# Performance work log

Hardware: AMD Instinct MI355X
Metric: run time of the kernel (lower is better)

Reference implementation:

```python
import jax, jax.numpy as jnp
import numpy as np
from jax import lax

STRIDES = (8, 16, 32)
NUM_CLASSES = 80
TOPK = 1000
CONF_THRESH = 0.05
NMS_THRESH = 0.6


def setup_inputs() -> dict:
    key = jax.random.key(0)
    ks = jax.random.split(key, 10)
    hw = [(256, 256), (128, 128), (64, 64)]
    inp = {}
    for lv, (h, w) in enumerate(hw):
        inp[f"cls_pred_{lv}"] = jax.random.normal(ks[3 * lv + 0], (NUM_CLASSES, h, w), jnp.float32)
        inp[f"reg_pred_{lv}"] = jax.random.normal(ks[3 * lv + 1], (4, h, w), jnp.float32)
        inp[f"ctn_pred_{lv}"] = jax.random.normal(ks[3 * lv + 2], (1, h, w), jnp.float32)
    inp["scales"] = jax.random.uniform(ks[9], (3,), jnp.float32)
    return inp


def _level_decode(cls_p, reg_p, ctn_p, scale, stride):
    # cls_p: [C,H,W] -> flatten to [M,C] matching torch permute(1,2,0).view(-1,C)
    C, H, W = cls_p.shape
    cls = jnp.transpose(cls_p, (1, 2, 0)).reshape(-1, C)          # [M,C]
    reg = jnp.transpose(reg_p, (1, 2, 0)).reshape(-1, 4)          # [M,4]
    reg = jax.nn.relu(reg * scale) * stride                       # Scale + relu + stride
    ctn = jnp.transpose(ctn_p, (1, 2, 0)).reshape(-1, 1)          # [M,1]
    joint = jnp.sqrt(jax.nn.sigmooid(cls) * jax.nn.sigmoid(ctn)) if False else \
        jnp.sqrt(jax.nn.sigmoid(cls) * jax.nn.sigmoid(ctn))      # [M,C]
    scores = jnp.max(joint, axis=-1)                              # [M]
    labels = jnp.argmax(joint, axis=-1)                           # [M]
    ay, ax = jnp.meshgrid(jnp.arange(H), jnp.arange(W), indexing='ij')
    anchors = (jnp.stack([ax, ay], -1).reshape(-1, 2).astype(cls.dtype) + 0.5) * stride  # [M,2]
    # per-level topk (M > TOPK for all levels here)
    scores, idx = lax.top_k(scores, TOPK)
    labels = labels[idx]
    reg = reg[idx]
    anchors = anchors[idx]
    boxes = jnp.concatenate([anchors - reg[:, :2], anchors + reg[:, 2:]], axis=-1)  # x1y1x2y2
    return scores, labels, boxes


def _nms(boxes, scores):
    # Faithful port of the pure-python NMS: fixed-shape keep mask, sorted order.
    N = boxes.shape[0]
    order = jnp.argsort(-scores)
    b = boxes[order]
    x1, y1, x2, y2 = b[:, 0], b[:, 1], b[:, 2], b[:, 3]
    areas = (x2 - x1) * (y2 - y1)
    xx1 = jnp.maximum(x1[:, None], x1[None, :])
    yy1 = jnp.maximum(y1[:, None], y1[None, :])
    xx2 = jnp.minimum(x2[:, None], x2[None, :])
    yy2 = jnp.minimum(y2[:, None], y2[None, :])
    w = jnp.maximum(1e-10, xx2 - xx1)
    h = jnp.maximum(1e-10, yy2 - yy1)
    inter = w * h
    iou = inter / (areas[:, None] + areas[None, :] - inter + 1e-14)  # [N,N]
    idxs = jnp.arange(N)

    def body(i, keep):
        sup = (iou[i] > NMS_THRESH) & (idxs > i) & keep[i]
        return keep & ~sup

    keep = lax.fori_loop(0, N, body, jnp.ones((N,), bool))
    return order, keep


def reference(cls_pred_0, cls_pred_1, cls_pred_2,
              reg_pred_0, reg_pred_1, reg_pred_2,
              ctn_pred_0, ctn_pred_1, ctn_pred_2, scales):
    cls_l = [cls_pred_0, cls_pred_1, cls_pred_2]
    reg_l = [reg_pred_0, reg_pred_1, reg_pred_2]
    ctn_l = [ctn_pred_0, ctn_pred_1, ctn_pred_2]
    all_s, all_l, all_b = [], [], []
    for lv in range(3):
        s, lb, bx = _level_decode(cls_l[lv], reg_l[lv], ctn_l[lv], scales[lv], float(STRIDES[lv]))
        all_s.append(s); all_l.append(lb); all_b.append(bx)
    scores = jnp.concatenate(all_s)   # [3000]
    labels = jnp.concatenate(all_l)
    boxes = jnp.concatenate(all_b)    # [3000,4]
    order, keep = _nms(boxes, scores)
    scores_s = scores[order]
    labels_s = labels[order]
    boxes_s = boxes[order]
    keep = keep & (scores_s > CONF_THRESH)
    return boxes_s, scores_s, labels_s, keep
```

## Files before the change

### kernel.cpp

```cpp
#include <hip/hip_runtime.h>
#include <cmath>
#include <stdint.h>

#define NPTS   86016
#define NB     (1 << 18)
#define NCB    1024
#define K_TOP  1000
#define NOUT   3000
#define NWORDS 47
#define NTILE  47
#define CAND_CAP 16384
#define ECAP   8192
#define FCAP   1024
#define SPPB   64

#define HIST_OFF   0
#define CH_OFF     (NB * 3 * 4)
#define CNT_OFF    (CH_OFF + NCB * 3 * 4)
#define MEMSET_BYTES (CNT_OFF + 64)
#define KEYS_OFF   (CNT_OFF + 64)
#define LAB_OFF    (KEYS_OFF + NPTS * 8)
#define SURE_OFF   (LAB_OFF + NPTS * 4)
#define CAND_OFF   (SURE_OFF + 3 * 1024 * 8)
#define SURV_OFF   (CAND_OFF + 3 * CAND_CAP * 8)
#define EDGE_OFF   (SURV_OFF + NOUT * 8 + 64)
#define FLAG_OFF   (EDGE_OFF + ECAP * 4)

__device__ __forceinline__ float sig_f32_stepwise(float x) {
    float e = (float)exp(-(double)x);
    return 1.0f / (1.0f + e);
}

__device__ __forceinline__ void locate(int g, int& lv, int& p, int& HW) {
    if (g < 65536)      { lv = 0; p = g;         HW = 65536; }
    else if (g < 81920) { lv = 1; p = g - 65536; HW = 16384; }
    else                { lv = 2; p = g - 81920; HW = 4096;  }
}

__global__ __launch_bounds__(256) void score_kernel(
        const float* __restrict__ cls0, const float* __restrict__ cls1,
        const float* __restrict__ cls2,
        const float* __restrict__ ctn0, const float* __restrict__ ctn1,
        const float* __restrict__ ctn2,
        unsigned long long* __restrict__ keys, int* __restrict__ labels,
        int* __restrict__ hist, int* __restrict__ chist,
        int* __restrict__ cnt, unsigned* __restrict__ flags) {
    __shared__ float pm[5 * SPPB], pv[5 * SPPB];
    __shared__ int pidx[5 * SPPB];
    __shared__ int lch[NCB];
    const int tid = threadIdx.x;
    const int base = blockIdx.x * SPPB;
    for (int i = tid; i < NCB; i += 256) lch[i] = 0;
    for (int it = tid; it < 5 * SPPB; it += 256) {
        int c = it / SPPB, pt = it - c * SPPB;
        int g = base + pt, lv, p, HW;
        locate(g, lv, p, HW);
        const float* cls = (lv == 0) ? cls0 : ((lv == 1) ? cls1 : cls2);
        const float* bp = cls + (size_t)c * 16 * HW + p;
        float x[16];
#pragma unroll
        for (int cc = 0; cc < 16; cc++) x[cc] = bp[(size_t)cc * HW];
        float m = -INFINITY, v = -INFINITY; int idx = 0;
#pragma unroll
        for (int cc = 0; cc < 16; cc++)
            if (x[cc] > m) { v = m; m = x[cc]; idx = c * 16 + cc; }
        pm[it] = m; pv[it] = v; pidx[it] = idx;
    }
    __syncthreads();
    if (tid < SPPB) {
        int g = base + tid, lv, p, HW;
        locate(g, lv, p, HW);
        const float* ctn = (lv == 0) ? ctn0 : ((lv == 1) ? ctn1 : ctn2);
        float m = -INFINITY, v = -INFINITY; int idx = 0;
#pragma unroll
        for (int k = 0; k < 5; k++) {
            float bm = pm[k * SPPB + tid];
            float bv = pv[k * SPPB + tid];
            int bidx = pidx[k * SPPB + tid];
            if (bm > m) { v = fmaxf(m, bv); m = bm; idx = bidx; }
        }
        float sc = sig_f32_stepwise(ctn[p]);
        float sM = sig_f32_stepwise(m);
        float jm = __fsqrt_rn(sM * sc);
        float sV = sig_f32_stepwise(v);
        float jv = __fsqrt_rn(sV * sc);
        if (jv == jm) {
            int f = atomicAdd(&cnt[13], 1);
            if (f < FCAP) flags[f] = (unsigned)g;
        }
        unsigned int bits = __float_as_uint(jm);
        keys[g] = ((unsigned long long)bits << 32) | (0xFFFFFFFFu - (unsigned)g);
        labels[g] = idx;
        atomicAdd(&hist[lv * NB + (int)(bits >> 12)], 1);
        atomicAdd(&lch[(int)(bits >> 20)], 1);
    }
    __syncthreads();
    int lv0, p0, HW0; locate(base, lv0, p0, HW0);
    for (int i = tid; i < NCB; i += 256) {
        int v = lch[i];
        if (v) atomicAdd(&chist[lv0 * NCB + i], v);
    }
}

__global__ __launch_bounds__(1024) void thresh_kernel(
        const float* __restrict__ cls0, const float* __restrict__ cls1,
        const float* __restrict__ cls2,
        const float* __restrict__ ctn0, const float* __restrict__ ctn1,
        const float* __restrict__ ctn2,
        const int* __restrict__ hist, const int* __restrict__ chist,
        int* __restrict__ cnt,
        const unsigned* __restrict__ flags, int* __restrict__ labels) {
    int bid = blockIdx.x, tid = threadIdx.x;
    if (bid < 3) {
        int lv = bid;
        const int* h = hist + lv * NB;
        __shared__ int part[1024];
        __shared__ int s_chunk, s_above;
        __shared__ int bins[257];
        part[tid] = chist[lv * NCB + tid];
        __syncthreads();
        for (int off = 1; off < 1024; off <<= 1) {
            int v = part[tid] + ((tid + off < 1024) ? part[tid + off] : 0);
            __syncthreads(); part[tid] = v; __syncthreads();
        }
        int nxt = (tid < 1023) ? part[tid + 1] : 0;
        if (part[tid] >= K_TOP && nxt < K_TOP) { s_chunk = tid; s_above = nxt; }
        __syncthreads();
        int chunk = s_chunk, above = s_above;
        if (tid < 256) bins[tid] = h[chunk * 256 + tid];
        __syncthreads();
        for (int off = 1; off < 256; off <<= 1) {
            int v = 0;
            if (tid < 256) v = bins[tid] + ((tid + off < 256) ? bins[tid + off] : 0);
            __syncthreads(); if (tid < 256) bins[tid] = v; __syncthreads();
        }
        if (tid < 256) {
            int ge    = above + bins[tid];
            int genxt = above + ((tid < 255) ? bins[tid + 1] : 0);
            if (ge >= K_TOP && genxt < K_TOP) {
                cnt[6 + lv] = chunk * 256 + tid;
                cnt[9 + lv] = K_TOP - genxt;
            }
        }
    } else {
        int nf = cnt[13]; if (nf > FCAP) nf = FCAP;
        int wave = tid >> 6, lane = tid & 63;
        for (int f = wave; f < nf; f += 16) {
            int g = (int)flags[f], lv, p, HW;
            locate(g, lv, p, HW);
            const float* cls = (lv == 0) ? cls0 : ((lv == 1) ? cls1 : cls2);
            const float* ctn = (lv == 0) ? ctn0 : ((lv == 1) ? ctn1 : ctn2);
            float sc = sig_f32_stepwise(ctn[p]);
            float bestv = -1.0f; int besti = 127;
            {
                float s = sig_f32_stepwise(cls[(size_t)lane * HW + p]);
                float sj = __fsqrt_rn(s * sc);
                bestv = sj; besti = lane;
            }
            if (lane < 16) {
                int c2 = lane + 64;
                float s = sig_f32_stepwise(cls[(size_t)c2 * HW + p]);
                float sj = __fsqrt_rn(s * sc);
                if (sj > bestv) { bestv = sj; besti = c2; }
            }
            for (int off = 32; off; off >>= 1) {
                float ov = __shfl_xor(bestv, off, 64);
                int   oi = __shfl_xor(besti, off, 64);
                if (ov > bestv || (ov == bestv && oi < besti)) { bestv = ov; besti = oi; }
            }
            if (lane == 0) labels[g] = besti;
        }
    }
}

__global__ void compact_kernel(const unsigned long long* __restrict__ keys,
                               int* __restrict__ cnt,
                               unsigned long long* __restrict__ sure,
                               unsigned long long* __restrict__ cand) {
    int g = blockIdx.x * blockDim.x + threadIdx.x;
    if (g >= NPTS) return;
    int lv = (g < 65536) ? 0 : (g < 81920 ? 1 : 2);
    unsigned long long key = keys[g];
    int bin = (int)(key >> 44);
    int B = cnt[6 + lv];
    if (bin > B) {
        int i = atomicAdd(&cnt[0 + lv], 1);
        sure[lv * 1024 + i] = key;
    } else if (bin == B) {
        int i = atomicAdd(&cnt[3 + lv], 1);
        if (i < CAND_CAP) cand[lv * CAND_CAP + i] = key;
    }
}

__global__ void select_kernel(const int* __restrict__ cnt,
                              const unsigned long long* __restrict__ sure,
                              unsigned long long* __restrict__ cand,
                              unsigned long long* __restrict__ surv) {
    int lv = blockIdx.x, tid = threadIdx.x;
    unsigned long long* c = cand + lv * CAND_CAP;
    int n = cnt[3 + lv]; if (n > CAND_CAP) n = CAND_CAP;
    int R = cnt[9 + lv];
    int Ca = K_TOP - R;
    int m = 1; while (m < n) m <<= 1;
    for (int t = n + tid; t < m; t += 1024) c[t] = 0ULL;
    __syncthreads();
    for (int k = 2; k <= m; k <<= 1)
        for (int j = k >> 1; j > 0; j >>= 1) {
            for (int t = tid; t < m; t += 1024) {
                int l = t ^ j;
                if (l > t) {
                    unsigned long long a = c[t], b = c[l];
                    if (((t & k) == 0) ? (a < b) : (a > b)) { c[t] = b; c[l] = a; }
                }
            }
            __syncthreads();
        }
    __shared__ unsigned long long s[1024];
    s[tid] = (tid < Ca) ? sure[lv * 1024 + tid]
                        : ((tid < K_TOP) ? c[tid - Ca] : 0ULL);
    __syncthreads();
    for (int k = 2; k <= 1024; k <<= 1)
        for (int j = k >> 1; j > 0; j >>= 1) {
            int l = tid ^ j;
            if (l > tid) {
                unsigned long long a = s[tid], b = s[l];
                if (((tid & k) == 0) ? (a < b) : (a > b)) { s[tid] = b; s[l] = a; }
            }
            __syncthreads();
        }
    if (tid < K_TOP) surv[lv * K_TOP + tid] = s[tid];
}

__global__ __launch_bounds__(1024) void merge_emit_kernel(
        const unsigned long long* __restrict__ surv,
        const int* __restrict__ labels,
        const float* __restrict__ reg0, const float* __restrict__ reg1,
        const float* __restrict__ reg2,
        const float* __restrict__ scales,
        float* __restrict__ out) {
    __shared__ unsigned long long L[3][1024];
    __shared__ unsigned long long s[NOUT];
    int tid = threadIdx.x;
#pragma unroll
    for (int lv = 0; lv < 3; lv++)
        L[lv][tid] = (tid < K_TOP) ? surv[lv * K_TOP + tid] : 0ULL;
    __syncthreads();
    for (int e = tid; e < NOUT; e += 1024) {
        int a = e / K_TOP, i = e - a * K_TOP;
        unsigned long long key = L[a][i];
        int rank = i;
#pragma unroll
        for (int b = 0; b < 3; b++) {
            if (b == a) continue;
            int lo = 0, hi = K_TOP;
            while (lo < hi) {
                int mid = (lo + hi) >> 1;
                if (L[b][mid] > key) lo = mid + 1; else hi = mid;
            }
            rank += lo;
        }
        s[rank] = key;
    }
    __syncthreads();
    for (int r = tid; r < NOUT; r += 1024) {
        unsigned long long key = s[r];
        unsigned int bits = (unsigned)(key >> 32);
        float score = __uint_as_float(bits);
        unsigned int g = 0xFFFFFFFFu - (unsigned)(key & 0xFFFFFFFFULL);
        int lv, p;
        if (g < 65536u)      { lv = 0; p = (int)g; }
        else if (g < 81920u) { lv = 1; p = (int)g - 65536; }
        else                 { lv = 2; p = (int)g - 81920; }
        const float* rp = (lv == 0) ? reg0 : ((lv == 1) ? reg1 : reg2);
        int HW = (lv == 0) ? 65536 : ((lv == 1) ? 16384 : 4096);
        int W = 256 >> lv;
        float strideF = (float)(8 << lv);
        float scale = scales[lv];
        int x = p & (W - 1);
        int y = p >> (8 - lv);
        float r0 = fmaxf(0.0f, rp[0 * HW + p] * scale) * strideF;
        float r1 = fmaxf(0.0f, rp[1 * HW + p] * scale) * strideF;
        float r2 = fmaxf(0.0f, rp[2 * HW + p] * scale) * strideF;
        float r3 = fmaxf(0.0f, rp[3 * HW + p] * scale) * strideF;
        float ax = ((float)x + 0.5f) * strideF;
        float ay = ((float)y + 0.5f) * strideF;
        out[r * 4 + 0] = ax - r0;
        out[r * 4 + 1] = ay - r1;
        out[r * 4 + 2] = ax + r2;
        out[r * 4 + 3] = ay + r3;
        out[12000 + r] = score;
        out[15000 + r] = (float)labels[g];
    }
}

__global__ __launch_bounds__(256) void edge_kernel(const float* __restrict__ out,
                                                   unsigned* __restrict__ edges_g,
                                                   int* __restrict__ cnt) {
    __shared__ float x1[128], y1[128], x2[128], y2[128];
    int t = blockIdx.x, tid = threadIdx.x;
    int ta = 0, rem = t;
    while (rem >= NTILE - ta) { rem -= NTILE - ta; ta++; }
    int tb = ta + rem;
    if (tid < 64) {
        int gi = ta * 64 + tid;
        if (gi < NOUT) {
            float4 b = ((const float4*)out)[gi];
            x1[tid] = b.x; y1[tid] = b.y; x2[tid] = b.z; y2[tid] = b.w;
        }
    } else if (tid < 128) {
        int gj = tb * 64 + (tid - 64);
        if (gj < NOUT) {
            float4 b = ((const float4*)out)[gj];
            x1[tid] = b.x; y1[tid] = b.y; x2[tid] = b.z; y2[tid] = b.w;
        }
    }
    __syncthreads();
#pragma unroll
    for (int q = 0; q < 16; q++) {
        int idx = q * 256 + tid;
        int ii = idx >> 6, jj = idx & 63;
        int i = ta * 64 + ii, j = tb * 64 + jj;
        if (i < j && j < NOUT) {
            float ai = (x2[ii] - x1[ii]) * (y2[ii] - y1[ii]);
            float aj = (x2[64 + jj] - x1[64 + jj]) * (y2[64 + jj] - y1[64 + jj]);
            float xx1 = fmaxf(x1[ii], x1[64 + jj]), yy1 = fmaxf(y1[ii], y1[64 + jj]);
            float xx2 = fminf(x2[ii], x2[64 + jj]), yy2 = fminf(y2[ii], y2[64 + jj]);
            float ww = fmaxf(1e-10f, xx2 - xx1);
            float hh = fmaxf(1e-10f, yy2 - yy1);
            float inter = ww * hh;
            float iou = inter / (((ai + aj) - inter) + 1e-14f);
            if ((double)iou > 0.6) {
                int e = atomicAdd(&cnt[12], 1);
                if (e < ECAP) edges_g[e] = ((unsigned)i << 12) | (unsigned)j;
            }
        }
    }
}

__global__ __launch_bounds__(1024) void nms_sparse_kernel(
        const unsigned* __restrict__ edges_g,
        const int* __restrict__ cnt,
        const float* __restrict__ scores_s,
        float* __restrict__ keep_out) {
    __shared__ unsigned ed[ECAP];
    __shared__ unsigned long long supLds[NWORDS];
    int tid = threadIdx.x;
    int E = cnt[12]; if (E > ECAP) E = ECAP;
    int m = 1; while (m < E) m <<= 1;
    for (int t = tid; t < m; t += 1024) ed[t] = (t < E) ? edges_g[t] : 0xFFFFFFFFu;
    __syncthreads();
    for (int k = 2; k <= m; k <<= 1)
        for (int j = k >> 1; j > 0; j >>= 1) {
            for (int t = tid; t < m; t += 1024) {
                int l = t ^ j;
                if (l > t) {
                    unsigned a = ed[t], b = ed[l];
                    if (((t & k) == 0) ? (a > b) : (a < b)) { ed[t] = b; ed[l] = a; }
                }
            }
            __syncthreads();
        }
    if (tid < 64) {
        int lane = tid;
        unsigned long long supW = 0ULL;
        int ep = 0;
        for (int c = 0; c < NWORDS; c++) {
            unsigned long long cw = __shfl(supW, c, 64);
            int hi = (c + 1) * 64;
            while (ep < E) {
                unsigned k = ed[ep];
                int i = (int)(k >> 12);
                if (i >= hi) break;
                int j = (int)(k & 4095);
                if (!((cw >> (i & 63)) & 1ULL)) {
                    if ((j >> 6) == c) cw |= 1ULL << (j & 63);
                    else if (lane == (j >> 6)) supW |= 1ULL << (j & 63);
                }
                ep++;
            }
            if (lane == c) supW = cw;
        }
        if (lane < NWORDS) supLds[lane] = supW;
    }
    __syncthreads();
    for (int j = tid; j < NOUT; j += 1024) {
        bool s = (supLds[j >> 6] >> (j & 63)) & 1ULL;
        float scv = scores_s[j];
        keep_out[j] = (!s && ((double)scv > 0.05)) ? 1.0f : 0.0f;
    }
}

extern "C" void kernel_launch(void* const* d_in, const int* in_sizes, int n_in,
                              void* d_out, int out_size, void* d_ws, size_t ws_size,
                              hipStream_t stream) {
    const float* cls0 = (const float*)d_in[0];
    const float* reg0 = (const float*)d_in[1];
    const float* ctn0 = (const float*)d_in[2];
    const float* cls1 = (const float*)d_in[3];
    const float* reg1 = (const float*)d_in[4];
    const float* ctn1 = (const float*)d_in[5];
    const float* cls2 = (const float*)d_in[6];
    const float* reg2 = (const float*)d_in[7];
    const float* ctn2 = (const float*)d_in[8];
    const float* scales = (const float*)d_in[9];

    char* ws = (char*)d_ws;
    int* hist = (int*)(ws + HIST_OFF);
    int* chist = (int*)(ws + CH_OFF);
    int* cnt  = (int*)(ws + CNT_OFF);
    unsigned long long* keys = (unsigned long long*)(ws + KEYS_OFF);
    int* labels = (int*)(ws + LAB_OFF);
    unsigned long long* sure = (unsigned long long*)(ws + SURE_OFF);
    unsigned long long* cand = (unsigned long long*)(ws + CAND_OFF);
    unsigned long long* surv = (unsigned long long*)(ws + SURV_OFF);
    unsigned* edges = (unsigned*)(ws + EDGE_OFF);
    unsigned* flags = (unsigned*)(ws + FLAG_OFF);
    float* out = (float*)d_out;

    hipMemsetAsync(ws, 0, MEMSET_BYTES, stream);

    score_kernel<<<NPTS / SPPB, 256, 0, stream>>>(cls0, cls1, cls2, ctn0, ctn1, ctn2,
                                                  keys, labels, hist, chist, cnt, flags);
    thresh_kernel<<<4, 1024, 0, stream>>>(cls0, cls1, cls2, ctn0, ctn1, ctn2,
                                          hist, chist, cnt, flags, labels);
    compact_kernel<<<(NPTS + 255) / 256, 256, 0, stream>>>(keys, cnt, sure, cand);
    select_kernel<<<3, 1024, 0, stream>>>(cnt, sure, cand, surv);
    merge_emit_kernel<<<1, 1024, 0, stream>>>(surv, labels, reg0, reg1, reg2, scales, out);
    edge_kernel<<<NTILE * (NTILE + 1) / 2, 256, 0, stream>>>(out, edges, cnt);
    nms_sparse_kernel<<<1, 1024, 0, stream>>>(edges, cnt, out + 12000, out + 18000);
}
```

Before: 193.4 us.

## Vectorize score kernel and fuse threshold, compact, select and merge kernels

The score kernel now processes 1024 points per block, with each thread handling 4 adjacent points through float4 loads across all 80 classes, so the shared-memory two-stage reduction is gone. The per-level threshold search is now recomputed redundantly in every compact block and fused with the compaction, and the per-level select sort runs inside the single-block merge/emit kernel. This removes two kernel launches and the surv round trip through global memory. In exchange, 84 blocks each redo the histogram scan, and the three per-level bitonic sorts now run serially in one block instead of in three parallel blocks.

```diff
diff --git a/kernel.cpp b/kernel.cpp
--- a/kernel.cpp
+++ b/kernel.cpp
@@ -12,7 +12,7 @@
 #define CAND_CAP 16384
 #define ECAP   8192
 #define FCAP   1024
-#define SPPB   64
+#define PPB    1024
 
 #define HIST_OFF   0
 #define CH_OFF     (NB * 3 * 4)
@@ -22,8 +22,7 @@
 #define LAB_OFF    (KEYS_OFF + NPTS * 8)
 #define SURE_OFF   (LAB_OFF + NPTS * 4)
 #define CAND_OFF   (SURE_OFF + 3 * 1024 * 8)
-#define SURV_OFF   (CAND_OFF + 3 * CAND_CAP * 8)
-#define EDGE_OFF   (SURV_OFF + NOUT * 8 + 64)
+#define EDGE_OFF   (CAND_OFF + 3 * CAND_CAP * 8)
 #define FLAG_OFF   (EDGE_OFF + ECAP * 4)
 
 __device__ __forceinline__ float sig_f32_stepwise(float x) {
@@ -45,44 +44,47 @@
         unsigned long long* __restrict__ keys, int* __restrict__ labels,
         int* __restrict__ hist, int* __restrict__ chist,
         int* __restrict__ cnt, unsigned* __restrict__ flags) {
-    __shared__ float pm[5 * SPPB], pv[5 * SPPB];
-    __shared__ int pidx[5 * SPPB];
     __shared__ int lch[NCB];
     const int tid = threadIdx.x;
-    const int base = blockIdx.x * SPPB;
+    const int base = blockIdx.x * PPB;
     for (int i = tid; i < NCB; i += 256) lch[i] = 0;
-    for (int it = tid; it < 5 * SPPB; it += 256) {
-        int c = it / SPPB, pt = it - c * SPPB;
-        int g = base + pt, lv, p, HW;
-        locate(g, lv, p, HW);
-        const float* cls = (lv == 0) ? cls0 : ((lv == 1) ? cls1 : cls2);
-        const float* bp = cls + (size_t)c * 16 * HW + p;
-        float x[16];
-#pragma unroll
-        for (int cc = 0; cc < 16; cc++) x[cc] = bp[(size_t)cc * HW];
-        float m = -INFINITY, v = -INFINITY; int idx = 0;
+    __syncthreads();
+
+    int g0 = base + tid * 4;
+    int lv, p0, HW;
+    locate(g0, lv, p0, HW);
+    const float* cls = (lv == 0) ? cls0 : ((lv == 1) ? cls1 : cls2);
+    const float* ctn = (lv == 0) ? ctn0 : ((lv == 1) ? ctn1 : ctn2);
+
+    float4 m4 = make_float4(-INFINITY, -INFINITY, -INFINITY, -INFINITY);
+    float4 v4 = m4;
+    int4 idx4 = make_int4(0, 0, 0, 0);
+    for (int ch = 0; ch < 5; ch++) {
+        float4 x[16];
 #pragma unroll
         for (int cc = 0; cc < 16; cc++)
-            if (x[cc] > m) { v = m; m = x[cc]; idx = c * 16 + cc; }
-        pm[it] = m; pv[it] = v; pidx[it] = idx;
-    }
-    __syncthreads();
-    if (tid < SPPB) {
-        int g = base + tid, lv, p, HW;
-        locate(g, lv, p, HW);
-        const float* ctn = (lv == 0) ? ctn0 : ((lv == 1) ? ctn1 : ctn2);
-        float m = -INFINITY, v = -INFINITY; int idx = 0;
+            x[cc] = *(const float4*)(cls + (size_t)(ch * 16 + cc) * HW + p0);
 #pragma unroll
-        for (int k = 0; k < 5; k++) {
-            float bm = pm[k * SPPB + tid];
-            float bv = pv[k * SPPB + tid];
-            int bidx = pidx[k * SPPB + tid];
-            if (bm > m) { v = fmaxf(m, bv); m = bm; idx = bidx; }
-        }
-        float sc = sig_f32_stepwise(ctn[p]);
-        float sM = sig_f32_stepwise(m);
+        for (int cc = 0; cc < 16; cc++) {
+            int c = ch * 16 + cc;
+            if (x[cc].x > m4.x) { v4.x = m4.x; m4.x = x[cc].x; idx4.x = c; }
+            if (x[cc].y > m4.y) { v4.y = m4.y; m4.y = x[cc].y; idx4.y = c; }
+            if (x[cc].z > m4.z) { v4.z = m4.z; m4.z = x[cc].z; idx4.z = c; }
+            if (x[cc].w > m4.w) { v4.w = m4.w; m4.w = x[cc].w; idx4.w = c; }
+        }
+    }
+    float4 ct = *(const float4*)(ctn + p0);
+    float mq[4] = { m4.x, m4.y, m4.z, m4.w };
+    float vq[4] = { v4.x, v4.y, v4.z, v4.w };
+    int   iq[4] = { idx4.x, idx4.y, idx4.z, idx4.w };
+    float cq[4] = { ct.x, ct.y, ct.z, ct.w };
+#pragma unroll
+    for (int q = 0; q < 4; q++) {
+        int g = g0 + q;
+        float sc = sig_f32_stepwise(cq[q]);
+        float sM = sig_f32_stepwise(mq[q]);
         float jm = __fsqrt_rn(sM * sc);
-        float sV = sig_f32_stepwise(v);
+        float sV = sig_f32_stepwise(vq[q]);
         float jv = __fsqrt_rn(sV * sc);
         if (jv == jm) {
             int f = atomicAdd(&cnt[13], 1);
@@ -90,32 +92,33 @@
         }
         unsigned int bits = __float_as_uint(jm);
         keys[g] = ((unsigned long long)bits << 32) | (0xFFFFFFFFu - (unsigned)g);
-        labels[g] = idx;
+        labels[g] = iq[q];
         atomicAdd(&hist[lv * NB + (int)(bits >> 12)], 1);
         atomicAdd(&lch[(int)(bits >> 20)], 1);
     }
     __syncthreads();
-    int lv0, p0, HW0; locate(base, lv0, p0, HW0);
     for (int i = tid; i < NCB; i += 256) {
         int v = lch[i];
-        if (v) atomicAdd(&chist[lv0 * NCB + i], v);
-    }
-}
-
-__global__ __launch_bounds__(1024) void thresh_kernel(
+        if (v) atomicAdd(&chist[lv * NCB + i], v);
+    }
+}
+
+__global__ __launch_bounds__(1024) void compact_kernel(
         const float* __restrict__ cls0, const float* __restrict__ cls1,
         const float* __restrict__ cls2,
         const float* __restrict__ ctn0, const float* __restrict__ ctn1,
         const float* __restrict__ ctn2,
+        const unsigned long long* __restrict__ keys,
         const int* __restrict__ hist, const int* __restrict__ chist,
         int* __restrict__ cnt,
+        unsigned long long* __restrict__ sure, unsigned long long* __restrict__ cand,
         const unsigned* __restrict__ flags, int* __restrict__ labels) {
     int bid = blockIdx.x, tid = threadIdx.x;
-    if (bid < 3) {
-        int lv = bid;
-        const int* h = hist + lv * NB;
+    if (bid < NPTS / PPB) {
+        int base = bid * PPB;
+        int lv, pp, HW; locate(base, lv, pp, HW);
         __shared__ int part[1024];
-        __shared__ int s_chunk, s_above;
+        __shared__ int s_chunk, s_above, s_B;
         __shared__ int bins[257];
         part[tid] = chist[lv * NCB + tid];
         __syncthreads();
@@ -127,6 +130,7 @@
         if (part[tid] >= K_TOP && nxt < K_TOP) { s_chunk = tid; s_above = nxt; }
         __syncthreads();
         int chunk = s_chunk, above = s_above;
+        const int* h = hist + lv * NB;
         if (tid < 256) bins[tid] = h[chunk * 256 + tid];
         __syncthreads();
         for (int off = 1; off < 256; off <<= 1) {
@@ -138,9 +142,23 @@
             int ge    = above + bins[tid];
             int genxt = above + ((tid < 255) ? bins[tid + 1] : 0);
             if (ge >= K_TOP && genxt < K_TOP) {
-                cnt[6 + lv] = chunk * 256 + tid;
+                int B = chunk * 256 + tid;
+                s_B = B;
+                cnt[6 + lv] = B;
                 cnt[9 + lv] = K_TOP - genxt;
             }
+        }
+        __syncthreads();
+        int B = s_B;
+        int g = base + tid;
+        unsigned long long key = keys[g];
+        int bin = (int)(key >> 44);
+        if (bin > B) {
+            int i = atomicAdd(&cnt[0 + lv], 1);
+            sure[lv * 1024 + i] = key;
+        } else if (bin == B) {
+            int i = atomicAdd(&cnt[3 + lv], 1);
+            if (i < CAND_CAP) cand[lv * CAND_CAP + i] = key;
         }
     } else {
         int nf = cnt[13]; if (nf > FCAP) nf = FCAP;
@@ -173,66 +191,10 @@
     }
 }
 
-__global__ void compact_kernel(const unsigned long long* __restrict__ keys,
-                               int* __restrict__ cnt,
-                               unsigned long long* __restrict__ sure,
-                               unsigned long long* __restrict__ cand) {
-    int g = blockIdx.x * blockDim.x + threadIdx.x;
-    if (g >= NPTS) return;
-    int lv = (g < 65536) ? 0 : (g < 81920 ? 1 : 2);
-    unsigned long long key = keys[g];
-    int bin = (int)(key >> 44);
-    int B = cnt[6 + lv];
-    if (bin > B) {
-        int i = atomicAdd(&cnt[0 + lv], 1);
-        sure[lv * 1024 + i] = key;
-    } else if (bin == B) {
-        int i = atomicAdd(&cnt[3 + lv], 1);
-        if (i < CAND_CAP) cand[lv * CAND_CAP + i] = key;
-    }
-}
-
-__global__ void select_kernel(const int* __restrict__ cnt,
-                              const unsigned long long* __restrict__ sure,
-                              unsigned long long* __restrict__ cand,
-                              unsigned long long* __restrict__ surv) {
-    int lv = blockIdx.x, tid = threadIdx.x;
-    unsigned long long* c = cand + lv * CAND_CAP;
-    int n = cnt[3 + lv]; if (n > CAND_CAP) n = CAND_CAP;
-    int R = cnt[9 + lv];
-    int Ca = K_TOP - R;
-    int m = 1; while (m < n) m <<= 1;
-    for (int t = n + tid; t < m; t += 1024) c[t] = 0ULL;
-    __syncthreads();
-    for (int k = 2; k <= m; k <<= 1)
-        for (int j = k >> 1; j > 0; j >>= 1) {
-            for (int t = tid; t < m; t += 1024) {
-                int l = t ^ j;
-                if (l > t) {
-                    unsigned long long a = c[t], b = c[l];
-                    if (((t & k) == 0) ? (a < b) : (a > b)) { c[t] = b; c[l] = a; }
-                }
-            }
-            __syncthreads();
-        }
-    __shared__ unsigned long long s[1024];
-    s[tid] = (tid < Ca) ? sure[lv * 1024 + tid]
-                        : ((tid < K_TOP) ? c[tid - Ca] : 0ULL);
-    __syncthreads();
-    for (int k = 2; k <= 1024; k <<= 1)
-        for (int j = k >> 1; j > 0; j >>= 1) {
-            int l = tid ^ j;
-            if (l > tid) {
-                unsigned long long a = s[tid], b = s[l];
-                if (((tid & k) == 0) ? (a < b) : (a > b)) { s[tid] = b; s[l] = a; }
-            }
-            __syncthreads();
-        }
-    if (tid < K_TOP) surv[lv * K_TOP + tid] = s[tid];
-}
-
-__global__ __launch_bounds__(1024) void merge_emit_kernel(
-        const unsigned long long* __restrict__ surv,
+__global__ __launch_bounds__(1024) void selmerge_kernel(
+        const int* __restrict__ cnt,
+        const unsigned long long* __restrict__ sure,
+        unsigned long long* __restrict__ cand,
         const int* __restrict__ labels,
         const float* __restrict__ reg0, const float* __restrict__ reg1,
         const float* __restrict__ reg2,
@@ -240,11 +202,42 @@
         float* __restrict__ out) {
     __shared__ unsigned long long L[3][1024];
     __shared__ unsigned long long s[NOUT];
+    __shared__ unsigned long long s1[1024];
     int tid = threadIdx.x;
-#pragma unroll
-    for (int lv = 0; lv < 3; lv++)
-        L[lv][tid] = (tid < K_TOP) ? surv[lv * K_TOP + tid] : 0ULL;
-    __syncthreads();
+    for (int lv = 0; lv < 3; lv++) {
+        unsigned long long* c = cand + lv * CAND_CAP;
+        int n = cnt[3 + lv]; if (n > CAND_CAP) n = CAND_CAP;
+        int R = cnt[9 + lv];
+        int Ca = K_TOP - R;
+        int m = 1; while (m < n) m <<= 1;
+        for (int t = n + tid; t < m; t += 1024) c[t] = 0ULL;
+        __syncthreads();
+        for (int k = 2; k <= m; k <<= 1)
+            for (int j = k >> 1; j > 0; j >>= 1) {
+                for (int t = tid; t < m; t += 1024) {
+                    int l = t ^ j;
+                    if (l > t) {
+                        unsigned long long a = c[t], b = c[l];
+                        if (((t & k) == 0) ? (a < b) : (a > b)) { c[t] = b; c[l] = a; }
+                    }
+                }
+                __syncthreads();
+            }
+        s1[tid] = (tid < Ca) ? sure[lv * 1024 + tid]
+                             : ((tid < K_TOP) ? c[tid - Ca] : 0ULL);
+        __syncthreads();
+        for (int k = 2; k <= 1024; k <<= 1)
+            for (int j = k >> 1; j > 0; j >>= 1) {
+                int l = tid ^ j;
+                if (l > tid) {
+                    unsigned long long a = s1[tid], b = s1[l];
+                    if (((tid & k) == 0) ? (a < b) : (a > b)) { s1[tid] = b; s1[l] = a; }
+                }
+                __syncthreads();
+            }
+        L[lv][tid] = s1[tid];
+        __syncthreads();
+    }
     for (int e = tid; e < NOUT; e += 1024) {
         int a = e / K_TOP, i = e - a * K_TOP;
         unsigned long long key = L[a][i];
@@ -412,20 +405,19 @@
     int* labels = (int*)(ws + LAB_OFF);
     unsigned long long* sure = (unsigned long long*)(ws + SURE_OFF);
     unsigned long long* cand = (unsigned long long*)(ws + CAND_OFF);
-    unsigned long long* surv = (unsigned long long*)(ws + SURV_OFF);
     unsigned* edges = (unsigned*)(ws + EDGE_OFF);
     unsigned* flags = (unsigned*)(ws + FLAG_OFF);
     float* out = (float*)d_out;
 
     hipMemsetAsync(ws, 0, MEMSET_BYTES, stream);
 
-    score_kernel<<<NPTS / SPPB, 256, 0, stream>>>(cls0, cls1, cls2, ctn0, ctn1, ctn2,
-                                                  keys, labels, hist, chist, cnt, flags);
-    thresh_kernel<<<4, 1024, 0, stream>>>(cls0, cls1, cls2, ctn0, ctn1, ctn2,
-                                          hist, chist, cnt, flags, labels);
-    compact_kernel<<<(NPTS + 255) / 256, 256, 0, stream>>>(keys, cnt, sure, cand);
-    select_kernel<<<3, 1024, 0, stream>>>(cnt, sure, cand, surv);
-    merge_emit_kernel<<<1, 1024, 0, stream>>>(surv, labels, reg0, reg1, reg2, scales, out);
+    score_kernel<<<NPTS / PPB, 256, 0, stream>>>(cls0, cls1, cls2, ctn0, ctn1, ctn2,
+                                                 keys, labels, hist, chist, cnt, flags);
+    compact_kernel<<<NPTS / PPB + 1, 1024, 0, stream>>>(cls0, cls1, cls2, ctn0, ctn1, ctn2,
+                                                        keys, hist, chist, cnt,
+                                                        sure, cand, flags, labels);
+    selmerge_kernel<<<1, 1024, 0, stream>>>(cnt, sure, cand, labels,
+                                            reg0, reg1, reg2, scales, out);
     edge_kernel<<<NTILE * (NTILE + 1) / 2, 256, 0, stream>>>(out, edges, cnt);
     nms_sparse_kernel<<<1, 1024, 0, stream>>>(edges, cnt, out + 12000, out + 18000);
 }
```

Measured after the change: 198.1 us. 1.02x slower.
